# Kernel optimization log

Hardware: AMD Instinct MI355X
Metric: run time of the kernel (lower is better)

The kernel has to match this reference:

```python
import jax, jax.numpy as jnp
import numpy as np

LAYERS = 30
LPS = 10            # layers per stack (layers // stacks)
K = 3               # kernel size
RC = 64             # residual channels
GC = 128            # gate channels
SC = 64             # skip channels
AC = 80             # aux (mel) channels
DN = ('NCH', 'OIH', 'NCH')


def _conv1x1(w, x):
    # w: (O, I), x: (B, I, T) -> (B, O, T)
    return jnp.einsum('oi,bit->bot', w, x)


def setup_inputs() -> dict:
    key = jax.random.key(0)
    ks = jax.random.split(key, 10)
    B, T = 8, 8192
    s = 0.05
    f32 = jnp.float32
    inp = {
        'x': jax.random.normal(ks[0], (B, 1, T), f32),
        'x_mask': jnp.ones((B, 1, T), f32),
        'c': jax.random.normal(ks[1], (B, AC, T), f32),
        'first_w': jax.random.normal(ks[2], (RC, 1, 1), f32) * s,
        'first_b': jnp.zeros((RC,), f32),
        'conv_w': jax.random.normal(ks[3], (LAYERS, GC, RC, K), f32) * s,
        'conv_b': jnp.zeros((LAYERS, GC), f32),
        'aux_w': jax.random.normal(ks[4], (LAYERS, GC, AC), f32) * s,
        'out_w': jax.random.normal(ks[5], (LAYERS, RC + SC, GC // 2), f32) * s,
        'out_b': jnp.zeros((LAYERS, RC + SC), f32),
        'last_w1': jax.random.normal(ks[6], (SC, SC), f32) * s,
        'last_b1': jnp.zeros((SC,), f32),
        'last_w2': jax.random.normal(ks[7], (1, SC), f32) * s,
        'last_b2': jnp.zeros((1,), f32),
    }
    return inp


def reference(x, x_mask, c, first_w, first_b, conv_w, conv_b, aux_w,
              out_w, out_b, last_w1, last_b1, last_w2, last_b2):
    # first 1x1 conv: (B,1,T) -> (B,RC,T)
    x = jax.lax.conv_general_dilated(x, first_w, (1,), [(0, 0)],
                                     dimension_numbers=DN) + first_b[None, :, None]
    skips = jnp.zeros_like(x[:, :SC])  # (B, SC, T)
    for l in range(LAYERS):
        d = 2 ** (l % LPS)
        pad = (K - 1) // 2 * d
        residual = x
        # dilated conv (same padding): (B,RC,T) -> (B,GC,T)
        h = jax.lax.conv_general_dilated(x, conv_w[l], (1,), [(pad, pad)],
                                         rhs_dilation=(d,), dimension_numbers=DN)
        h = h + conv_b[l][None, :, None]
        # local conditioning 1x1 (no bias)
        h = h + _conv1x1(aux_w[l], c)
        xa, xb = jnp.split(h, 2, axis=1)          # (B, GC/2, T) each
        z = jnp.tanh(xa) * jax.nn.sigmoid(xb)     # gated activation
        o = _conv1x1(out_w[l], z) + out_b[l][None, :, None]  # (B, RC+SC, T)
        o = o * x_mask
        x = residual + o[:, :RC]
        skips = skips + o[:, RC:]
    # last_conv: ReLU -> 1x1 -> ReLU -> 1x1
    y = jax.nn.relu(skips)
    y = _conv1x1(last_w1, y) + last_b1[None, :, None]
    y = jax.nn.relu(y)
    y = _conv1x1(last_w2, y) + last_b2[None, :, None]
    return y
```

## Files before the change

kernel.cpp:

```cpp
#include <hip/hip_runtime.h>
#include <hip/hip_bf16.h>
#include <stdint.h>

#define T_LEN 8192
#define LAYERS 30

typedef __attribute__((ext_vector_type(8))) short bfx8;
typedef __attribute__((ext_vector_type(4))) float fx4;
typedef __attribute__((ext_vector_type(4))) int ix4;

static __device__ __forceinline__ unsigned short f2bf(float f) {
    union { float fv; unsigned u; } v; v.fv = f;
    unsigned r = v.u + 0x7fffu + ((v.u >> 16) & 1u);
    return (unsigned short)(r >> 16);
}
static __device__ __forceinline__ unsigned pack2(float a, float b) {
    return (unsigned)f2bf(a) | ((unsigned)f2bf(b) << 16);
}

__global__ void pack_weights_k(const float* __restrict__ conv_w,
                               const float* __restrict__ aux_w,
                               const float* __restrict__ out_w,
                               unsigned short* __restrict__ wpack) {
    int tid = blockIdx.x * 256 + threadIdx.x;
    int lane = tid & 63;
    int f = (tid >> 6) % 88;
    int l = tid / (88 * 64);
    unsigned short vals[8];
#pragma unroll
    for (int j = 0; j < 8; j++) {
        int kl = ((lane >> 4) * 8) + j;
        float v;
        if (f < 72) {
            int ks = f >> 3, nf = f & 7;
            int g = nf * 16 + (lane & 15);
            if (ks < 6) {
                int tap = ks >> 1;
                int i = (ks & 1) * 32 + kl;
                v = conv_w[((l * 128 + g) * 64 + i) * 3 + tap];
            } else {
                int a = (ks - 6) * 32 + kl;
                v = (a < 80) ? aux_w[(l * 128 + g) * 80 + a] : 0.f;
            }
        } else {
            int fo = f - 72;
            int ks = fo >> 3, nf = fo & 7;
            int p = nf * 16 + (lane & 15);
            v = out_w[(l * 128 + p) * 64 + ks * 32 + kl];
        }
        vals[j] = f2bf(v);
    }
    unsigned* dst = (unsigned*)(wpack + (size_t)tid * 8);
    dst[0] = (unsigned)vals[0] | ((unsigned)vals[1] << 16);
    dst[1] = (unsigned)vals[2] | ((unsigned)vals[3] << 16);
    dst[2] = (unsigned)vals[4] | ((unsigned)vals[5] << 16);
    dst[3] = (unsigned)vals[6] | ((unsigned)vals[7] << 16);
}

__global__ void prep_c_k(const float* __restrict__ c, unsigned short* __restrict__ cbf) {
    __shared__ float tile[80][65];
    int bid = blockIdx.x;
    int b = bid >> 7;
    int t0 = (bid & 127) << 6;
    for (int idx = threadIdx.x; idx < 80 * 64; idx += 256) {
        int a = idx >> 6, tt = idx & 63;
        tile[a][tt] = c[((size_t)(b * 80 + a)) * T_LEN + t0 + tt];
    }
    __syncthreads();
    for (int idx = threadIdx.x; idx < 64 * 96; idx += 256) {
        int tt = idx / 96, a = idx % 96;
        float v = (a < 80) ? tile[a][tt] : 0.f;
        cbf[((size_t)(b * T_LEN + t0 + tt)) * 96 + a] = f2bf(v);
    }
}

__global__ void first_init_k(const float* __restrict__ x,
                             const float* __restrict__ fw, const float* __restrict__ fb,
                             float* __restrict__ xf32, unsigned short* __restrict__ xbf,
                             float* __restrict__ skip) {
    int vi = blockIdx.x * 256 + threadIdx.x;
    if (vi < 1048576) {
        int pos = vi >> 4;
        int rc = (vi & 15) * 4;
        float xs = x[pos];
        const float4 w = *(const float4*)(fw + rc);
        const float4 bb = *(const float4*)(fb + rc);
        float4 val = make_float4(w.x * xs + bb.x, w.y * xs + bb.y,
                                 w.z * xs + bb.z, w.w * xs + bb.w);
        *(float4*)(xf32 + (((size_t)pos) << 6) + rc) = val;
        unsigned* dst = (unsigned*)(xbf + (((size_t)pos) << 6) + rc);
        dst[0] = (unsigned)f2bf(val.x) | ((unsigned)f2bf(val.y) << 16);
        dst[1] = (unsigned)f2bf(val.z) | ((unsigned)f2bf(val.w) << 16);
    } else {
        int si = vi - 1048576;
        float4 z = make_float4(0.f, 0.f, 0.f, 0.f);
        *(float4*)(skip + (size_t)si * 4) = z;
    }
}

__global__ __launch_bounds__(256, 4) void layer_k(
    const unsigned short* __restrict__ xbf_cur,
    unsigned short* __restrict__ xbf_next,
    float* __restrict__ xf32,
    float* __restrict__ skip,
    const unsigned short* __restrict__ cbf,
    const float* __restrict__ xmask,
    const unsigned short* __restrict__ wl,
    const float* __restrict__ conv_b_l,
    const float* __restrict__ out_b_l,
    int d)
{
    __shared__ char smem[40960];
    unsigned short* xtap  = (unsigned short*)smem;
    float*          sg_l  = (float*)smem;
    unsigned short* z_l   = (unsigned short*)(smem + 17408);
    float*          o_l   = (float*)smem;
    unsigned short* ctile = (unsigned short*)(smem + 27648);

    const int tid = threadIdx.x;
    const int lane = tid & 63;
    const int wv = tid >> 6;
    int bid = (((int)blockIdx.x & 7) * 128) + ((int)blockIdx.x >> 3);
    const int b = bid >> 7;
    const int t0 = (bid & 127) << 6;
    const long rowbase = (long)b * T_LEN;
    const int klane = (lane >> 4) * 8;
    const int mrow = lane & 15;
    const int trow = (lane >> 4) * 4;

    for (int idx = tid; idx < 1536; idx += 256) {
        int tap = idx >> 9, rem = idx & 511, row = rem >> 3, seg = rem & 7;
        int tg = t0 + row + (tap - 1) * d;
        ix4 v = {0, 0, 0, 0};
        if ((unsigned)tg < (unsigned)T_LEN)
            v = *(const ix4*)(xbf_cur + ((rowbase + tg) << 6) + seg * 8);
        *(ix4*)(xtap + (tap * 64 + row) * 72 + seg * 8) = v;
    }
    for (int idx = tid; idx < 768; idx += 256) {
        int row = idx / 12, seg = idx % 12;
        ix4 v = *(const ix4*)(cbf + (rowbase + t0 + row) * 96 + seg * 8);
        *(ix4*)(ctile + row * 104 + seg * 8) = v;
    }

    bfx8 bq[2][2];
#pragma unroll
    for (int pk = 0; pk < 2; pk++)
#pragma unroll
        for (int n = 0; n < 2; n++)
            bq[pk][n] = *(const bfx8*)(wl + (size_t)((pk * 8 + wv * 2 + n) * 64 + lane) * 8);
    __syncthreads();

    fx4 acc[4][2];
#pragma unroll
    for (int m = 0; m < 4; m++) {
        acc[m][0] = (fx4){0.f, 0.f, 0.f, 0.f};
        acc[m][1] = (fx4){0.f, 0.f, 0.f, 0.f};
    }
#pragma unroll
    for (int ks = 0; ks < 9; ks++) {
        const unsigned short* abase; int off, stride;
        if (ks < 6) { abase = xtap + (ks >> 1) * (64 * 72); off = (ks & 1) * 32; stride = 72; }
        else        { abase = ctile;                        off = (ks - 6) * 32; stride = 104; }
        bfx8 af[4];
#pragma unroll
        for (int m = 0; m < 4; m++)
            af[m] = *(const bfx8*)(abase + (m * 16 + mrow) * stride + off + klane);
        bfx8 b0 = bq[ks & 1][0], b1 = bq[ks & 1][1];
        if (ks + 2 < 9) {
#pragma unroll
            for (int n = 0; n < 2; n++)
                bq[ks & 1][n] = *(const bfx8*)(wl + (size_t)(((ks + 2) * 8 + wv * 2 + n) * 64 + lane) * 8);
        }
#pragma unroll
        for (int m = 0; m < 4; m++) {
            acc[m][0] = __builtin_amdgcn_mfma_f32_16x16x32_bf16(af[m], b0, acc[m][0], 0, 0, 0);
            acc[m][1] = __builtin_amdgcn_mfma_f32_16x16x32_bf16(af[m], b1, acc[m][1], 0, 0, 0);
        }
    }
    __syncthreads();

    {
        float cb0 = conv_b_l[wv * 32 + mrow];
        float cb1 = conv_b_l[wv * 32 + 16 + mrow];
        if (wv >= 2) {
#pragma unroll
            for (int n = 0; n < 2; n++) {
                int col = (wv - 2) * 32 + n * 16 + mrow;
                float cb = n ? cb1 : cb0;
#pragma unroll
                for (int m = 0; m < 4; m++)
#pragma unroll
                    for (int r = 0; r < 4; r++) {
                        float h = acc[m][n][r] + cb;
                        sg_l[(m * 16 + trow + r) * 68 + col] = 1.f / (1.f + __expf(-h));
                    }
            }
        } else {
#pragma unroll
            for (int n = 0; n < 2; n++) {
                float cb = n ? cb1 : cb0;
#pragma unroll
                for (int m = 0; m < 4; m++)
#pragma unroll
                    for (int r = 0; r < 4; r++) {
                        float h = acc[m][n][r] + cb;
                        float e2 = __expf(2.f * h);
                        acc[m][n][r] = 1.f - 2.f / (e2 + 1.f);
                    }
            }
        }
    }
    __syncthreads();

    bfx8 ob[2][2];
#pragma unroll
    for (int ks = 0; ks < 2; ks++)
#pragma unroll
        for (int n = 0; n < 2; n++)
            ob[ks][n] = *(const bfx8*)(wl + (size_t)(((72 + ks * 8) + (wv * 2 + n)) * 64 + lane) * 8);

    if (wv < 2) {
#pragma unroll
        for (int n = 0; n < 2; n++) {
            int col = wv * 32 + n * 16 + mrow;
#pragma unroll
            for (int m = 0; m < 4; m++)
#pragma unroll
                for (int r = 0; r < 4; r++) {
                    int t = m * 16 + trow + r;
                    z_l[t * 72 + col] = f2bf(acc[m][n][r] * sg_l[t * 68 + col]);
                }
        }
    }
    __syncthreads();

    fx4 acc2[4][2];
#pragma unroll
    for (int m = 0; m < 4; m++) {
        acc2[m][0] = (fx4){0.f, 0.f, 0.f, 0.f};
        acc2[m][1] = (fx4){0.f, 0.f, 0.f, 0.f};
    }
#pragma unroll
    for (int ks = 0; ks < 2; ks++) {
        bfx8 af[4];
#pragma unroll
        for (int m = 0; m < 4; m++)
            af[m] = *(const bfx8*)(z_l + (m * 16 + mrow) * 72 + ks * 32 + klane);
#pragma unroll
        for (int m = 0; m < 4; m++) {
            acc2[m][0] = __builtin_amdgcn_mfma_f32_16x16x32_bf16(af[m], ob[ks][0], acc2[m][0], 0, 0, 0);
            acc2[m][1] = __builtin_amdgcn_mfma_f32_16x16x32_bf16(af[m], ob[ks][1], acc2[m][1], 0, 0, 0);
        }
    }
    __syncthreads();

#pragma unroll
    for (int n = 0; n < 2; n++) {
        int p = wv * 32 + n * 16 + mrow;
        float ob_ = out_b_l[p];
#pragma unroll
        for (int m = 0; m < 4; m++)
#pragma unroll
            for (int r = 0; r < 4; r++) {
                int t = m * 16 + trow + r;
                o_l[t * 132 + p] = acc2[m][n][r] + ob_;
            }
    }
    __syncthreads();

    {
        int t = tid >> 2;
        int q = tid & 3;
        float mk = xmask[rowbase + t0 + t];
        const float* src = o_l + t * 132 + q * 32;
        long ro = (rowbase + t0 + t) << 6;
        if (q < 2) {
            float* xp = xf32 + ro + q * 32;
            unsigned short* bp = xbf_next + ro + q * 32;
            unsigned pk[16];
#pragma unroll
            for (int k = 0; k < 8; k++) {
                float4 o4 = *(const float4*)(src + k * 4);
                float4 xv = *(float4*)(xp + k * 4);
                xv.x = fmaf(o4.x, mk, xv.x); xv.y = fmaf(o4.y, mk, xv.y);
                xv.z = fmaf(o4.z, mk, xv.z); xv.w = fmaf(o4.w, mk, xv.w);
                *(float4*)(xp + k * 4) = xv;
                pk[k * 2]     = pack2(xv.x, xv.y);
                pk[k * 2 + 1] = pack2(xv.z, xv.w);
            }
#pragma unroll
            for (int k = 0; k < 4; k++)
                *(ix4*)(bp + k * 8) = *(const ix4*)(pk + k * 4);
        } else {
            float* sp = skip + ro + (q - 2) * 32;
#pragma unroll
            for (int k = 0; k < 8; k++) {
                float4 o4 = *(const float4*)(src + k * 4);
                float4 sv = *(float4*)(sp + k * 4);
                sv.x = fmaf(o4.x, mk, sv.x); sv.y = fmaf(o4.y, mk, sv.y);
                sv.z = fmaf(o4.z, mk, sv.z); sv.w = fmaf(o4.w, mk, sv.w);
                *(float4*)(sp + k * 4) = sv;
            }
        }
    }
}

__global__ __launch_bounds__(256) void final_k(
        const float* __restrict__ skip,
        const float* __restrict__ w1, const float* __restrict__ b1,
        const float* __restrict__ w2, const float* __restrict__ b2,
        float* __restrict__ out) {
    __shared__ float w1s[4096];
    __shared__ float b1s[64];
    __shared__ float w2s[64];
    for (int i = threadIdx.x; i < 4096; i += 256) w1s[i] = w1[i];
    if (threadIdx.x < 64) {
        b1s[threadIdx.x] = b1[threadIdx.x];
        w2s[threadIdx.x] = w2[threadIdx.x];
    }
    __syncthreads();

    int pos = blockIdx.x * 256 + threadIdx.x;
    const float4* row = (const float4*)(skip + (size_t)pos * 64);
    float4 s[16];
#pragma unroll
    for (int j = 0; j < 16; j++) {
        float4 v = row[j];
        s[j] = make_float4(fmaxf(v.x, 0.f), fmaxf(v.y, 0.f),
                           fmaxf(v.z, 0.f), fmaxf(v.w, 0.f));
    }
    float total = b2[0];
    for (int o = 0; o < 64; o++) {
        const float4* wr = (const float4*)(w1s + o * 64);
        float d0 = 0.f, d1 = 0.f, d2 = 0.f, d3 = 0.f;
#pragma unroll
        for (int j = 0; j < 16; j++) {
            float4 w = wr[j];
            d0 = fmaf(w.x, s[j].x, d0);
            d1 = fmaf(w.y, s[j].y, d1);
            d2 = fmaf(w.z, s[j].z, d2);
            d3 = fmaf(w.w, s[j].w, d3);
        }
        float dot = (d0 + d1) + (d2 + d3) + b1s[o];
        total = fmaf(w2s[o], fmaxf(dot, 0.f), total);
    }
    out[pos] = total;
}

extern "C" void kernel_launch(void* const* d_in, const int* in_sizes, int n_in,
                              void* d_out, int out_size, void* d_ws, size_t ws_size,
                              hipStream_t stream) {
    const float* x       = (const float*)d_in[0];
    const float* xmask   = (const float*)d_in[1];
    const float* c       = (const float*)d_in[2];
    const float* first_w = (const float*)d_in[3];
    const float* first_b = (const float*)d_in[4];
    const float* conv_w  = (const float*)d_in[5];
    const float* conv_b  = (const float*)d_in[6];
    const float* aux_w   = (const float*)d_in[7];
    const float* out_w   = (const float*)d_in[8];
    const float* out_b   = (const float*)d_in[9];
    const float* lw1     = (const float*)d_in[10];
    const float* lb1     = (const float*)d_in[11];
    const float* lw2     = (const float*)d_in[12];
    const float* lb2     = (const float*)d_in[13];
    float* out = (float*)d_out;

    char* ws = (char*)d_ws;
    float*          xf32  = (float*)(ws + 0);
    unsigned short* xbfA  = (unsigned short*)(ws + 16777216);
    unsigned short* xbfB  = (unsigned short*)(ws + 25165824);
    float*          skip  = (float*)(ws + 33554432);
    unsigned short* cbf   = (unsigned short*)(ws + 50331648);
    unsigned short* wpack = (unsigned short*)(ws + 62914560);

    pack_weights_k<<<660, 256, 0, stream>>>(conv_w, aux_w, out_w, wpack);
    prep_c_k<<<1024, 256, 0, stream>>>(c, cbf);
    first_init_k<<<8192, 256, 0, stream>>>(x, first_w, first_b, xf32, xbfA, skip);

    const unsigned short* cur = xbfA;
    unsigned short* nxt = xbfB;
    for (int l = 0; l < LAYERS; l++) {
        int d = 1 << (l % 10);
        layer_k<<<1024, 256, 0, stream>>>(cur, nxt, xf32, skip, cbf, xmask,
                                          wpack + (size_t)l * 45056,
                                          conv_b + l * 128, out_b + l * 128, d);
        const unsigned short* tmp = nxt;
        nxt = (unsigned short*)cur;
        cur = tmp;
    }
    final_k<<<256, 256, 0, stream>>>(skip, lw1, lb1, lw2, lb2, out);
}
```

Baseline: 963.2 us.

## Fuse first conv into layer kernel, read fp32 residual directly, store skip as bf16

Removes the separate init kernel by computing the first 1x1 conv inside layer 0. Each layer now reads the fp32 residual with taps and converts it to bf16 in shared memory, instead of keeping a separate bf16 copy. The residual ping-pongs between two fp32 buffers. Skip accumulation is stored in bf16, which halves skip traffic but accumulates rounding error across 30 layers. Tap loads now fetch fp32, so each tap read moves twice the bytes, while the bf16 x write and the separate xf32 read-modify-write go away.

New measurement: 795.1 us. 1.21x faster.

```diff
diff --git a/kernel.cpp b/kernel.cpp
--- a/kernel.cpp
+++ b/kernel.cpp
@@ -13,6 +13,10 @@
     union { float fv; unsigned u; } v; v.fv = f;
     unsigned r = v.u + 0x7fffu + ((v.u >> 16) & 1u);
     return (unsigned short)(r >> 16);
+}
+static __device__ __forceinline__ float bf2f(unsigned short u) {
+    union { unsigned u; float f; } v; v.u = ((unsigned)u) << 16;
+    return v.f;
 }
 static __device__ __forceinline__ unsigned pack2(float a, float b) {
     return (unsigned)f2bf(a) | ((unsigned)f2bf(b) << 16);
@@ -74,41 +78,17 @@
     }
 }
 
-__global__ void first_init_k(const float* __restrict__ x,
-                             const float* __restrict__ fw, const float* __restrict__ fb,
-                             float* __restrict__ xf32, unsigned short* __restrict__ xbf,
-                             float* __restrict__ skip) {
-    int vi = blockIdx.x * 256 + threadIdx.x;
-    if (vi < 1048576) {
-        int pos = vi >> 4;
-        int rc = (vi & 15) * 4;
-        float xs = x[pos];
-        const float4 w = *(const float4*)(fw + rc);
-        const float4 bb = *(const float4*)(fb + rc);
-        float4 val = make_float4(w.x * xs + bb.x, w.y * xs + bb.y,
-                                 w.z * xs + bb.z, w.w * xs + bb.w);
-        *(float4*)(xf32 + (((size_t)pos) << 6) + rc) = val;
-        unsigned* dst = (unsigned*)(xbf + (((size_t)pos) << 6) + rc);
-        dst[0] = (unsigned)f2bf(val.x) | ((unsigned)f2bf(val.y) << 16);
-        dst[1] = (unsigned)f2bf(val.z) | ((unsigned)f2bf(val.w) << 16);
-    } else {
-        int si = vi - 1048576;
-        float4 z = make_float4(0.f, 0.f, 0.f, 0.f);
-        *(float4*)(skip + (size_t)si * 4) = z;
-    }
-}
-
 __global__ __launch_bounds__(256, 4) void layer_k(
-    const unsigned short* __restrict__ xbf_cur,
-    unsigned short* __restrict__ xbf_next,
-    float* __restrict__ xf32,
-    float* __restrict__ skip,
+    const float* __restrict__ xsrc,
+    float* __restrict__ xdst,
+    unsigned short* __restrict__ skipbf,
     const unsigned short* __restrict__ cbf,
     const float* __restrict__ xmask,
+    const float* __restrict__ fw, const float* __restrict__ fb,
     const unsigned short* __restrict__ wl,
     const float* __restrict__ conv_b_l,
     const float* __restrict__ out_b_l,
-    int d)
+    int d, int first)
 {
     __shared__ char smem[40960];
     unsigned short* xtap  = (unsigned short*)smem;
@@ -127,14 +107,63 @@
     const int klane = (lane >> 4) * 8;
     const int mrow = lane & 15;
     const int trow = (lane >> 4) * 4;
-
-    for (int idx = tid; idx < 1536; idx += 256) {
-        int tap = idx >> 9, rem = idx & 511, row = rem >> 3, seg = rem & 7;
-        int tg = t0 + row + (tap - 1) * d;
-        ix4 v = {0, 0, 0, 0};
-        if ((unsigned)tg < (unsigned)T_LEN)
-            v = *(const ix4*)(xbf_cur + ((rowbase + tg) << 6) + seg * 8);
-        *(ix4*)(xtap + (tap * 64 + row) * 72 + seg * 8) = v;
+    const int tq_t = tid >> 2;
+    const int tq_q = tid & 3;
+
+    float xc[16];
+    if (first) {
+        float xs = xsrc[rowbase + t0 + tq_t];
+#pragma unroll
+        for (int k = 0; k < 16; k++)
+            xc[k] = fmaf(fw[tq_q * 16 + k], xs, fb[tq_q * 16 + k]);
+    } else {
+        const float4* src = (const float4*)(xsrc + ((rowbase + t0 + tq_t) << 6) + tq_q * 16);
+#pragma unroll
+        for (int k = 0; k < 4; k++) {
+            float4 v = src[k];
+            xc[k * 4] = v.x; xc[k * 4 + 1] = v.y; xc[k * 4 + 2] = v.z; xc[k * 4 + 3] = v.w;
+        }
+    }
+    {
+        unsigned pk[8];
+#pragma unroll
+        for (int k = 0; k < 8; k++) pk[k] = pack2(xc[k * 2], xc[k * 2 + 1]);
+        unsigned short* dst = xtap + (64 + tq_t) * 72 + tq_q * 16;
+        *(ix4*)dst       = *(const ix4*)&pk[0];
+        *(ix4*)(dst + 8) = *(const ix4*)&pk[4];
+    }
+#pragma unroll
+    for (int u = 0; u < 2; u++) {
+        int idx = tid + u * 256;
+        int tp = idx >> 8;
+        int rem = idx & 255;
+        int row = rem >> 2, qq = rem & 3;
+        int tg = t0 + row + (tp ? d : -d);
+        float hv[16];
+        if ((unsigned)tg < (unsigned)T_LEN) {
+            if (first) {
+                float xs = xsrc[rowbase + tg];
+#pragma unroll
+                for (int k = 0; k < 16; k++)
+                    hv[k] = fmaf(fw[qq * 16 + k], xs, fb[qq * 16 + k]);
+            } else {
+                const float4* src = (const float4*)(xsrc + ((rowbase + tg) << 6) + qq * 16);
+#pragma unroll
+                for (int k = 0; k < 4; k++) {
+                    float4 v = src[k];
+                    hv[k * 4] = v.x; hv[k * 4 + 1] = v.y; hv[k * 4 + 2] = v.z; hv[k * 4 + 3] = v.w;
+                }
+            }
+        } else {
+#pragma unroll
+            for (int k = 0; k < 16; k++) hv[k] = 0.f;
+        }
+        unsigned pk[8];
+#pragma unroll
+        for (int k = 0; k < 8; k++) pk[k] = pack2(hv[k * 2], hv[k * 2 + 1]);
+        unsigned short* dst = xtap + (tp * 128 + row) * 72 + qq * 16;
+        *(ix4*)dst       = *(const ix4*)&pk[0];
+        *(ix4*)(dst + 8) = *(const ix4*)&pk[4];
     }
     for (int idx = tid; idx < 768; idx += 256) {
         int row = idx / 12, seg = idx % 12;
@@ -269,44 +298,48 @@
     __syncthreads();
 
     {
-        int t = tid >> 2;
-        int q = tid & 3;
-        float mk = xmask[rowbase + t0 + t];
-        const float* src = o_l + t * 132 + q * 32;
-        long ro = (rowbase + t0 + t) << 6;
-        if (q < 2) {
-            float* xp = xf32 + ro + q * 32;
-            unsigned short* bp = xbf_next + ro + q * 32;
-            unsigned pk[16];
-#pragma unroll
-            for (int k = 0; k < 8; k++) {
-                float4 o4 = *(const float4*)(src + k * 4);
-                float4 xv = *(float4*)(xp + k * 4);
-                xv.x = fmaf(o4.x, mk, xv.x); xv.y = fmaf(o4.y, mk, xv.y);
-                xv.z = fmaf(o4.z, mk, xv.z); xv.w = fmaf(o4.w, mk, xv.w);
-                *(float4*)(xp + k * 4) = xv;
-                pk[k * 2]     = pack2(xv.x, xv.y);
-                pk[k * 2 + 1] = pack2(xv.z, xv.w);
-            }
-#pragma unroll
-            for (int k = 0; k < 4; k++)
-                *(ix4*)(bp + k * 8) = *(const ix4*)(pk + k * 4);
+        float mk = xmask[rowbase + t0 + tq_t];
+        long ro = (rowbase + t0 + tq_t) << 6;
+        const float* osrc = o_l + tq_t * 132;
+        float* xp = xdst + ro + tq_q * 16;
+#pragma unroll
+        for (int k2 = 0; k2 < 4; k2++) {
+            float4 o4 = *(const float4*)(osrc + tq_q * 16 + k2 * 4);
+            float4 xv;
+            xv.x = fmaf(o4.x, mk, xc[k2 * 4 + 0]);
+            xv.y = fmaf(o4.y, mk, xc[k2 * 4 + 1]);
+            xv.z = fmaf(o4.z, mk, xc[k2 * 4 + 2]);
+            xv.w = fmaf(o4.w, mk, xc[k2 * 4 + 3]);
+            *(float4*)(xp + k2 * 4) = xv;
+        }
+        unsigned short* sp = skipbf + ro + tq_q * 16;
+        float sv[16];
+        if (first) {
+#pragma unroll
+            for (int k = 0; k < 16; k++)
+                sv[k] = osrc[64 + tq_q * 16 + k] * mk;
         } else {
-            float* sp = skip + ro + (q - 2) * 32;
-#pragma unroll
-            for (int k = 0; k < 8; k++) {
-                float4 o4 = *(const float4*)(src + k * 4);
-                float4 sv = *(float4*)(sp + k * 4);
-                sv.x = fmaf(o4.x, mk, sv.x); sv.y = fmaf(o4.y, mk, sv.y);
-                sv.z = fmaf(o4.z, mk, sv.z); sv.w = fmaf(o4.w, mk, sv.w);
-                *(float4*)(sp + k * 4) = sv;
-            }
-        }
+            ix4 old0 = *(const ix4*)sp;
+            ix4 old1 = *(const ix4*)(sp + 8);
+            const unsigned short* op = (const unsigned short*)&old0;
+            const unsigned short* op1 = (const unsigned short*)&old1;
+#pragma unroll
+            for (int k = 0; k < 8; k++)
+                sv[k] = fmaf(osrc[64 + tq_q * 16 + k], mk, bf2f(op[k]));
+#pragma unroll
+            for (int k = 0; k < 8; k++)
+                sv[8 + k] = fmaf(osrc[64 + tq_q * 16 + 8 + k], mk, bf2f(op1[k]));
+        }
+        unsigned pk[8];
+#pragma unroll
+        for (int k = 0; k < 8; k++) pk[k] = pack2(sv[k * 2], sv[k * 2 + 1]);
+        *(ix4*)sp       = *(const ix4*)&pk[0];
+        *(ix4*)(sp + 8) = *(const ix4*)&pk[4];
     }
 }
 
 __global__ __launch_bounds__(256) void final_k(
-        const float* __restrict__ skip,
+        const unsigned short* __restrict__ skipbf,
         const float* __restrict__ w1, const float* __restrict__ b1,
         const float* __restrict__ w2, const float* __restrict__ b2,
         float* __restrict__ out) {
@@ -321,13 +354,16 @@
     __syncthreads();
 
     int pos = blockIdx.x * 256 + threadIdx.x;
-    const float4* row = (const float4*)(skip + (size_t)pos * 64);
+    const ix4* rowp = (const ix4*)(skipbf + (size_t)pos * 64);
     float4 s[16];
 #pragma unroll
-    for (int j = 0; j < 16; j++) {
-        float4 v = row[j];
-        s[j] = make_float4(fmaxf(v.x, 0.f), fmaxf(v.y, 0.f),
-                           fmaxf(v.z, 0.f), fmaxf(v.w, 0.f));
+    for (int j = 0; j < 8; j++) {
+        ix4 v = rowp[j];
+        const unsigned short* pv = (const unsigned short*)&v;
+        s[j * 2]     = make_float4(fmaxf(bf2f(pv[0]), 0.f), fmaxf(bf2f(pv[1]), 0.f),
+                                   fmaxf(bf2f(pv[2]), 0.f), fmaxf(bf2f(pv[3]), 0.f));
+        s[j * 2 + 1] = make_float4(fmaxf(bf2f(pv[4]), 0.f), fmaxf(bf2f(pv[5]), 0.f),
+                                   fmaxf(bf2f(pv[6]), 0.f), fmaxf(bf2f(pv[7]), 0.f));
     }
     float total = b2[0];
     for (int o = 0; o < 64; o++) {
@@ -367,27 +403,25 @@
     float* out = (float*)d_out;
 
     char* ws = (char*)d_ws;
-    float*          xf32  = (float*)(ws + 0);
-    unsigned short* xbfA  = (unsigned short*)(ws + 16777216);
-    unsigned short* xbfB  = (unsigned short*)(ws + 25165824);
-    float*          skip  = (float*)(ws + 33554432);
-    unsigned short* cbf   = (unsigned short*)(ws + 50331648);
-    unsigned short* wpack = (unsigned short*)(ws + 62914560);
+    float*          xfA    = (float*)(ws + 0);
+    float*          xfB    = (float*)(ws + 16777216);
+    unsigned short* skipbf = (unsigned short*)(ws + 33554432);
+    unsigned short* cbf    = (unsigned short*)(ws + 41943040);
+    unsigned short* wpack  = (unsigned short*)(ws + 54525952);
 
     pack_weights_k<<<660, 256, 0, stream>>>(conv_w, aux_w, out_w, wpack);
     prep_c_k<<<1024, 256, 0, stream>>>(c, cbf);
-    first_init_k<<<8192, 256, 0, stream>>>(x, first_w, first_b, xf32, xbfA, skip);
-
-    const unsigned short* cur = xbfA;
-    unsigned short* nxt = xbfB;
+
+    const float* src = x;
     for (int l = 0; l < LAYERS; l++) {
         int d = 1 << (l % 10);
-        layer_k<<<1024, 256, 0, stream>>>(cur, nxt, xf32, skip, cbf, xmask,
+        float* dst = (l & 1) ? xfB : xfA;
+        layer_k<<<1024, 256, 0, stream>>>(src, dst, skipbf, cbf, xmask,
+                                          first_w, first_b,
                                           wpack + (size_t)l * 45056,
-                                          conv_b + l * 128, out_b + l * 128, d);
-        const unsigned short* tmp = nxt;
-        nxt = (unsigned short*)cur;
-        cur = tmp;
-    }
-    final_k<<<256, 256, 0, stream>>>(skip, lw1, lb1, lw2, lb2, out);
-}
+                                          conv_b + l * 128, out_b + l * 128,
+                                          d, (l == 0) ? 1 : 0);
+        src = dst;
+    }
+    final_k<<<256, 256, 0, stream>>>(skipbf, lw1, lb1, lw2, lb2, out);
+}
```
